# Kernel tuning notes

Measured on AMD Instinct MI355X. Metric: run time of the kernel, lower is better.

The kernel has to match this reference:

```python
import jax, jax.numpy as jnp
import numpy as np
import math

B, T, H, W, D = 64, 512, 128, 128, 32


def _lin(k, out, inn):
    k1, k2 = jax.random.split(k)
    lim = 1.0 / np.sqrt(inn)
    return (jax.random.uniform(k1, (out, inn), jnp.float32, -lim, lim),
            jax.random.uniform(k2, (out,), jnp.float32, -lim, lim))


def setup_inputs() -> dict:
    key = jax.random.key(0)
    ks = jax.random.split(key, 12)
    ts = jnp.broadcast_to(jnp.linspace(0.0, 4.0 * math.pi, T, dtype=jnp.float32), (B, T))
    coef = lambda k: jax.random.normal(k, (B, T - 1, D), jnp.float32) * 0.1
    i_W0, i_b0 = _lin(ks[4], W, D)
    i_W1, i_b1 = _lin(ks[5], W, W)
    i_W2, i_b2 = _lin(ks[6], H, W)
    f_W0, f_b0 = _lin(ks[7], W, H)
    f_W1, f_b1 = _lin(ks[8], W, W)
    f_W2, f_b2 = _lin(ks[9], H * D, W)
    l_W, l_b = _lin(ks[10], 1, H)
    return dict(ts=ts,
                coeff_d=coef(ks[0]), coeff_c=coef(ks[1]), coeff_b=coef(ks[2]), coeff_a=coef(ks[3]),
                i_W0=i_W0, i_b0=i_b0, i_W1=i_W1, i_b1=i_b1, i_W2=i_W2, i_b2=i_b2,
                f_W0=f_W0, f_b0=f_b0, f_W1=f_W1, f_b1=f_b1, f_W2=f_W2, f_b2=f_b2,
                l_W=l_W, l_b=l_b)


def reference(ts, coeff_d, coeff_c, coeff_b, coeff_a,
              i_W0, i_b0, i_W1, i_b1, i_W2, i_b2,
              f_W0, f_b0, f_W1, f_b1, f_W2, f_b2,
              l_W, l_b):
    def initial_mlp(x):  # eqx.nn.MLP default: relu hidden, identity final
        x = jax.nn.relu(i_W0 @ x + i_b0)
        x = jax.nn.relu(i_W1 @ x + i_b1)
        return i_W2 @ x + i_b2

    def func_mlp(y):  # softplus hidden, tanh final, reshape (H, D)
        h = jax.nn.softplus(f_W0 @ y + f_b0)
        h = jax.nn.softplus(f_W1 @ h + f_b1)
        return jnp.tanh(f_W2 @ h + f_b2).reshape(H, D)

    def single(ts_i, d, c, b, a):
        dt = ts_i[1] - ts_i[0]
        y0 = initial_mlp(a[0])  # control.evaluate(ts[0]) = a[0] (frac=0 in first interval)

        def deriv(t):  # diffrax CubicInterpolation.derivative
            idx = jnp.clip(jnp.searchsorted(ts_i, t, side='right') - 1, 0, ts_i.shape[0] - 2)
            frac = t - ts_i[idx]
            return b[idx] + frac * (2.0 * c[idx] + frac * 3.0 * d[idx])

        def f(t, y):  # ControlTerm.to_ode() vf_prod with control=dt
            return (func_mlp(y) @ deriv(t)) * dt

        def step(carry, _):  # ralston_step_fn
            t0, y = carry
            k1 = f(t0, y)
            k2 = f(t0 + 0.5 * dt, y + 0.5 * k1)
            k3 = f(t0 + 0.75 * dt, y + 0.75 * k2)
            y1 = (2.0 / 9.0 * k1 + 1.0 / 3.0 * k2 + 4.0 / 9.0 * k3) * dt + y
            return (t0 + dt, y1), y1

        _, ys = jax.lax.scan(step, (ts_i[0], y0), None, length=ts_i.shape[0])
        return jax.nn.sigmoid(ys @ l_W[0] + l_b[0])  # (T,), evolving_out=True

    return jax.vmap(single)(ts, coeff_d, coeff_c, coeff_b, coeff_a)
```

## Files before the change

### kernel.cpp

```cpp
#include <hip/hip_runtime.h>
#include <hip/hip_bf16.h>

#define TT 512
#define BB 64
#define HH 128
#define WW 128
#define DD 32
#define NTHR 512
#define CSTRIDE 16352

#define SMEM_BYTES 86016

typedef __attribute__((ext_vector_type(8))) short short8;
typedef __attribute__((ext_vector_type(4))) float f32x4;

__device__ __forceinline__ float softplus_f(float x) {
    return fmaxf(x, 0.f) + __logf(1.f + __expf(-fabsf(x)));
}
__device__ __forceinline__ float fast_tanh(float x) {
    float ax = fabsf(x);
    float e  = __expf(-2.f * ax);
    float r  = (1.f - e) * __builtin_amdgcn_rcpf(1.f + e);
    return copysignf(r, x);
}
__device__ __forceinline__ short bf16rne(float x) {
    unsigned u = __float_as_uint(x);
    u += 0x7fffu + ((u >> 16) & 1u);
    return (short)(u >> 16);
}
__device__ __forceinline__ void store_l2(unsigned long long* p, unsigned long long v) {
    asm volatile("global_store_dwordx2 %0, %1, off sc0"
                 :: "v"(p), "v"(v) : "memory");
}
__device__ __forceinline__ unsigned long long load_l2_atomic(unsigned long long* p) {
    unsigned long long v;
    asm volatile("global_atomic_add_x2 %0, %1, %2, off sc0\n\t"
                 "s_waitcnt vmcnt(0)"
                 : "=v"(v) : "v"(p), "v"(0ULL) : "memory");
    return v;
}

__global__ __launch_bounds__(NTHR, 2)
void cde_kernel(const float* __restrict__ ts,
                const float* __restrict__ cd, const float* __restrict__ cc,
                const float* __restrict__ cb, const float* __restrict__ ca,
                const float* __restrict__ iW0, const float* __restrict__ ib0,
                const float* __restrict__ iW1, const float* __restrict__ ib1,
                const float* __restrict__ iW2, const float* __restrict__ ib2,
                const float* __restrict__ fW0, const float* __restrict__ fb0,
                const float* __restrict__ fW1, const float* __restrict__ fb1,
                const float* __restrict__ fW2, const float* __restrict__ fb2,
                const float* __restrict__ lW, const float* __restrict__ lb,
                unsigned* __restrict__ xcdctr,
                float* camb,
                unsigned long long* kslow,
                float* __restrict__ out)
{
    extern __shared__ float sm[];
    float* tss    = sm;
    float* ybuf   = tss + TT;
    float* dvec   = ybuf + 128;
    float* scr    = dvec + 96;
    float* klocal = scr + 256;
    short* ybf    = (short*)(klocal + 32);
    short* h1bf   = ybf + 128;
    short* h2bf   = h1bf + 128;
    int*   clm    = (int*)(h2bf + 128);

    const int tid  = threadIdx.x;
    const int lane = tid & 63;
    const int wv   = tid >> 6;
    const int quad = lane >> 4;
    const int qr   = lane & 15;

    if (tid == 0) {
        unsigned xcc;
        asm volatile("s_getreg_b32 %0, hwreg(HW_REG_XCC_ID)" : "=s"(xcc));
        xcc &= 7u;
        unsigned slot = atomicAdd(&xcdctr[xcc], 1u);
        clm[0] = (int)(xcc * 8u + (slot >> 2));
        clm[1] = (int)(slot & 3u);
    }
    __syncthreads();
    const int b = clm[0];
    const int m = clm[1];

    unsigned long long* kfast =
        (unsigned long long*)(camb + (size_t)b * CSTRIDE + 2048);

    const int cg = qr & 3;
    const int ct = (qr >> 2) & 1;
    const int rh = qr >> 3;
    const int dbase = ct * 16 + quad * 4 + rh * 2;

    for (int i = tid; i < TT; i += NTHR) tss[i] = ts[(size_t)b * TT + i];

    short8 afr[4][8];
    #pragma unroll
    for (int gi = 0; gi < 4; ++gi) {
        int g = m * 32 + wv * 4 + gi;
        #pragma unroll
        for (int t = 0; t < 2; ++t)
        #pragma unroll
        for (int K = 0; K < 4; ++K) {
            int row = g * 32 + t * 16 + qr;
            int col = K * 32 + quad * 8;
            const float* src = fW2 + (size_t)row * WW + col;
            short8 v;
            #pragma unroll
            for (int j = 0; j < 8; ++j) v[j] = bf16rne(src[j]);
            afr[gi][t * 4 + K] = v;
        }
    }
    short8 w0f[4], w1f[4];
    #pragma unroll
    for (int K = 0; K < 4; ++K) {
        int row = wv * 16 + qr;
        int col = K * 32 + quad * 8;
        const float* s0 = fW0 + (size_t)row * HH + col;
        const float* s1 = fW1 + (size_t)row * WW + col;
        short8 v0, v1;
        #pragma unroll
        for (int j = 0; j < 8; ++j) { v0[j] = bf16rne(s0[j]); v1[j] = bf16rne(s1[j]); }
        w0f[K] = v0; w1f[K] = v1;
    }
    const float fb0r = fb0[wv * 16 + quad * 4 + cg];
    const float fb1r = fb1[wv * 16 + quad * 4 + cg];
    const int   hrow = m * 32 + wv * 4 + cg;
    const float fb2a = fb2[hrow * 32 + dbase];
    const float fb2b = fb2[hrow * 32 + dbase + 1];

    __syncthreads();

    const float dt = tss[1] - tss[0];
    float t00 = tss[0];
    const size_t cstride = (size_t)CSTRIDE;
    const float* cdb = cd + (size_t)b * cstride;
    const float* ccb = cc + (size_t)b * cstride;
    const float* cbb = cb + (size_t)b * cstride;

    if (tid < HH) {
        const float* a0 = ca + (size_t)b * cstride;
        float acc = ib0[tid];
        #pragma unroll
        for (int k = 0; k < DD; ++k) acc += iW0[tid * DD + k] * a0[k];
        scr[tid] = fmaxf(acc, 0.f);
    }
    __syncthreads();
    if (tid < HH) {
        float acc = ib1[tid];
        for (int k = 0; k < WW; ++k) acc += iW1[tid * WW + k] * scr[k];
        scr[128 + tid] = fmaxf(acc, 0.f);
    }
    __syncthreads();
    float yreg = 0.f, k1r = 0.f, k2r = 0.f;
    if (tid < HH) {
        float acc = ib2[tid];
        for (int k = 0; k < WW; ++k) acc += iW2[tid * WW + k] * scr[128 + k];
        yreg = acc;
        ybuf[tid] = acc;
        ybf[tid]  = bf16rne(acc);
    }
    __syncthreads();

    float lwa = 0.f, lwb = 0.f, lbv = 0.f;
    if (wv == 0) { lwa = lW[lane]; lwb = lW[64 + lane]; lbv = lb[0]; }

    for (int s = 0; s < TT; ++s) {
        if (wv < 3) {
            float tv = t00 + ((wv == 0) ? 0.f : (wv == 1) ? 0.5f : 0.75f) * dt;
            int cnt = 0;
            #pragma unroll
            for (int ch = 0; ch < 8; ++ch)
                cnt += __popcll(__ballot(tss[ch * 64 + lane] <= tv));
            int idx = min(max(cnt - 1, 0), TT - 2);
            if (lane < DD) {
                float frac = tv - tss[idx];
                size_t o = (size_t)idx * DD + lane;
                dvec[wv * 32 + lane] =
                    cbb[o] + frac * (2.f * ccb[o] + frac * 3.f * cdb[o]);
            }
        }

        #pragma unroll 1
        for (int q = 0; q < 3; ++q) {
            const int gen = s * 3 + q + 1;
            const int buf = gen & 1;

            {
                f32x4 aA = {0.f, 0.f, 0.f, 0.f}, aB = {0.f, 0.f, 0.f, 0.f};
                short8 b0 = *(const short8*)(ybf + 0 * 32 + quad * 8);
                short8 b1 = *(const short8*)(ybf + 1 * 32 + quad * 8);
                short8 b2 = *(const short8*)(ybf + 2 * 32 + quad * 8);
                short8 b3 = *(const short8*)(ybf + 3 * 32 + quad * 8);
                aA = __builtin_amdgcn_mfma_f32_16x16x32_bf16(w0f[0], b0, aA, 0, 0, 0);
                aB = __builtin_amdgcn_mfma_f32_16x16x32_bf16(w0f[1], b1, aB, 0, 0, 0);
                aA = __builtin_amdgcn_mfma_f32_16x16x32_bf16(w0f[2], b2, aA, 0, 0, 0);
                aB = __builtin_amdgcn_mfma_f32_16x16x32_bf16(w0f[3], b3, aB, 0, 0, 0);
                f32x4 h = aA + aB;
                if (qr < 4) {
                    float v = (qr & 1) ? ((qr & 2) ? h[3] : h[1])
                                       : ((qr & 2) ? h[2] : h[0]);
                    h1bf[wv * 16 + quad * 4 + qr] = bf16rne(softplus_f(v + fb0r));
                }
            }
            __syncthreads();
            {
                f32x4 aA = {0.f, 0.f, 0.f, 0.f}, aB = {0.f, 0.f, 0.f, 0.f};
                short8 b0 = *(const short8*)(h1bf + 0 * 32 + quad * 8);
                short8 b1 = *(const short8*)(h1bf + 1 * 32 + quad * 8);
                short8 b2 = *(const short8*)(h1bf + 2 * 32 + quad * 8);
                short8 b3 = *(const short8*)(h1bf + 3 * 32 + quad * 8);
                aA = __builtin_amdgcn_mfma_f32_16x16x32_bf16(w1f[0], b0, aA, 0, 0, 0);
                aB = __builtin_amdgcn_mfma_f32_16x16x32_bf16(w1f[1], b1, aB, 0, 0, 0);
                aA = __builtin_amdgcn_mfma_f32_16x16x32_bf16(w1f[2], b2, aA, 0, 0, 0);
                aB = __builtin_amdgcn_mfma_f32_16x16x32_bf16(w1f[3], b3, aB, 0, 0, 0);
                f32x4 h = aA + aB;
                if (qr < 4) {
                    float v = (qr & 1) ? ((qr & 2) ? h[3] : h[1])
                                       : ((qr & 2) ? h[2] : h[0]);
                    h2bf[wv * 16 + quad * 4 + qr] = bf16rne(softplus_f(v + fb1r));
                }
            }
            __syncthreads();

            {
                short8 bfr[4];
                #pragma unroll
                for (int K = 0; K < 4; ++K)
                    bfr[K] = *(const short8*)(h2bf + K * 32 + quad * 8);
                f32x4 A0[4], A1[4];
                #pragma unroll
                for (int gi = 0; gi < 4; ++gi) {
                    f32x4 a0 = {0.f, 0.f, 0.f, 0.f};
                    f32x4 a1 = {0.f, 0.f, 0.f, 0.f};
                    a0 = __builtin_amdgcn_mfma_f32_16x16x32_bf16(afr[gi][0], bfr[0], a0, 0, 0, 0);
                    a0 = __builtin_amdgcn_mfma_f32_16x16x32_bf16(afr[gi][1], bfr[1], a0, 0, 0, 0);
                    a0 = __builtin_amdgcn_mfma_f32_16x16x32_bf16(afr[gi][2], bfr[2], a0, 0, 0, 0);
                    a0 = __builtin_amdgcn_mfma_f32_16x16x32_bf16(afr[gi][3], bfr[3], a0, 0, 0, 0);
                    a1 = __builtin_amdgcn_mfma_f32_16x16x32_bf16(afr[gi][4], bfr[0], a1, 0, 0, 0);
                    a1 = __builtin_amdgcn_mfma_f32_16x16x32_bf16(afr[gi][5], bfr[1], a1, 0, 0, 0);
                    a1 = __builtin_amdgcn_mfma_f32_16x16x32_bf16(afr[gi][6], bfr[2], a1, 0, 0, 0);
                    a1 = __builtin_amdgcn_mfma_f32_16x16x32_bf16(afr[gi][7], bfr[3], a1, 0, 0, 0);
                    A0[gi] = a0; A1[gi] = a1;
                }
                f32x4 s0a = (cg & 1) ? A0[1] : A0[0];
                f32x4 s0b = (cg & 1) ? A0[3] : A0[2];
                f32x4 s0  = (cg & 2) ? s0b : s0a;
                f32x4 s1a = (cg & 1) ? A1[1] : A1[0];
                f32x4 s1b = (cg & 1) ? A1[3] : A1[2];
                f32x4 s1  = (cg & 2) ? s1b : s1a;
                f32x4 st  = ct ? s1 : s0;
                float va = rh ? st[2] : st[0];
                float vb = rh ? st[3] : st[1];
                float2 dv = *(const float2*)(dvec + q * 32 + dbase);
                float p = fast_tanh(va + fb2a) * dv.x + fast_tanh(vb + fb2b) * dv.y;
                p += __shfl_xor(p, 8);
                p += __shfl_xor(p, 4);
                p += __shfl_xor(p, 16);
                p += __shfl_xor(p, 32);
                if (lane < 4) {
                    const float kval = p * dt;
                    const size_t off = (size_t)buf * HH + m * 32 + wv * 4 + lane;
                    unsigned long long pk =
                        ((unsigned long long)__float_as_uint(kval) << 32) | (unsigned)gen;
                    klocal[wv * 4 + lane] = kval;
                    store_l2(kfast + off, pk);
                    __hip_atomic_store(&kslow[(size_t)(buf * BB + b) * HH + m * 32 + wv * 4 + lane],
                                       pk, __ATOMIC_RELAXED, __HIP_MEMORY_SCOPE_AGENT);
                }
            }
            __syncthreads();

            if (tid < HH) {
                float kv;
                const int rel = tid - m * 32;
                if (rel >= 0 && rel < 32) {
                    kv = klocal[rel];
                } else {
                    unsigned long long v;
                    int it = 0;
                    for (;;) {
                        if (it < 4 || (it & 1) == 0) {
                            v = load_l2_atomic(kfast + (size_t)buf * HH + tid);
                        } else {
                            v = __hip_atomic_load(&kslow[(size_t)(buf * BB + b) * HH + tid],
                                                  __ATOMIC_RELAXED, __HIP_MEMORY_SCOPE_AGENT);
                        }
                        if ((unsigned)v == (unsigned)gen) break;
                        if (++it > 64) __builtin_amdgcn_s_sleep(1);
                    }
                    kv = __uint_as_float((unsigned)(v >> 32));
                }
                float nxt;
                if (q == 0)      { k1r = kv; nxt = yreg + 0.5f  * kv; }
                else if (q == 1) { k2r = kv; nxt = yreg + 0.75f * kv; }
                else {
                    nxt = yreg + dt * ((2.f/9.f) * k1r + (1.f/3.f) * k2r + (4.f/9.f) * kv);
                    yreg = nxt;
                    ybuf[tid] = nxt;
                }
                ybf[tid] = bf16rne(nxt);
            }
            __syncthreads();
        }

        if (m == 0 && wv == 0) {
            float p = ybuf[lane] * lwa + ybuf[64 + lane] * lwb;
            p += __shfl_xor(p, 1);  p += __shfl_xor(p, 2);  p += __shfl_xor(p, 4);
            p += __shfl_xor(p, 8);  p += __shfl_xor(p, 16); p += __shfl_xor(p, 32);
            if (lane == 0) out[(size_t)b * TT + s] = 1.f / (1.f + __expf(-(p + lbv)));
        }
        t00 += dt;
    }
}

extern "C" void kernel_launch(void* const* d_in, const int* in_sizes, int n_in,
                              void* d_out, int out_size, void* d_ws, size_t ws_size,
                              hipStream_t stream) {
    const float* ts  = (const float*)d_in[0];
    const float* cdp = (const float*)d_in[1];
    const float* ccp = (const float*)d_in[2];
    const float* cbp = (const float*)d_in[3];
    const float* cap = (const float*)d_in[4];
    const float* iW0 = (const float*)d_in[5];
    const float* ib0 = (const float*)d_in[6];
    const float* iW1 = (const float*)d_in[7];
    const float* ib1 = (const float*)d_in[8];
    const float* iW2 = (const float*)d_in[9];
    const float* ib2 = (const float*)d_in[10];
    const float* fW0 = (const float*)d_in[11];
    const float* fb0 = (const float*)d_in[12];
    const float* fW1 = (const float*)d_in[13];
    const float* fb1 = (const float*)d_in[14];
    const float* fW2 = (const float*)d_in[15];
    const float* fb2 = (const float*)d_in[16];
    const float* lW  = (const float*)d_in[17];
    const float* lb  = (const float*)d_in[18];
    float* out = (float*)d_out;

    unsigned* xcdctr = (unsigned*)d_ws;
    unsigned long long* kslow = (unsigned long long*)((char*)d_ws + 256);
    hipMemsetAsync(d_ws, 0, 256 + (size_t)2 * BB * HH * sizeof(unsigned long long), stream);

    hipFuncSetAttribute((const void*)cde_kernel,
                        hipFuncAttributeMaxDynamicSharedMemorySize, SMEM_BYTES);
    hipLaunchKernelGGL(cde_kernel, dim3(256), dim3(NTHR), SMEM_BYTES, stream,
                       ts, cdp, ccp, cbp, cap, iW0, ib0, iW1, ib1, iW2, ib2,
                       fW0, fb0, fW1, fb1, fW2, fb2, lW, lb, xcdctr,
                       (float*)cap, kslow, out);
}
```

Before: 3.330 ms.

## Overlap cross-block k exchange with barrier and use lightweight LDS barriers

Replaces __syncthreads with an inline s_waitcnt lgkmcnt(0)+s_barrier so that outstanding global memory ops are not drained at each barrier. Consumers issue the first atomic probe of the foreign k value before the barrier and collect it afterwards, hiding part of the cross-block latency. The fallback kslow store is moved after the consumer step to get it off the critical path. The risk is memory-ordering subtleties, since global stores and loads are no longer fenced by the barrier.

```diff
diff --git a/kernel.cpp b/kernel.cpp
--- a/kernel.cpp
+++ b/kernel.cpp
@@ -28,6 +28,9 @@
     u += 0x7fffu + ((u >> 16) & 1u);
     return (short)(u >> 16);
 }
+__device__ __forceinline__ void lds_barrier() {
+    asm volatile("s_waitcnt lgkmcnt(0)\n\ts_barrier" ::: "memory");
+}
 __device__ __forceinline__ void store_l2(unsigned long long* p, unsigned long long v) {
     asm volatile("global_store_dwordx2 %0, %1, off sc0"
                  :: "v"(p), "v"(v) : "memory");
@@ -38,6 +41,13 @@
                  "s_waitcnt vmcnt(0)"
                  : "=v"(v) : "v"(p), "v"(0ULL) : "memory");
     return v;
+}
+__device__ __forceinline__ void probe_issue(unsigned long long* p, unsigned long long& v) {
+    asm volatile("global_atomic_add_x2 %0, %1, %2, off sc0"
+                 : "=v"(v) : "v"(p), "v"(0ULL) : "memory");
+}
+__device__ __forceinline__ void probe_collect(unsigned long long& v) {
+    asm volatile("s_waitcnt vmcnt(0)" : "+v"(v) :: "memory");
 }
 
 __global__ __launch_bounds__(NTHR, 2)
@@ -166,6 +176,10 @@
     float lwa = 0.f, lwb = 0.f, lbv = 0.f;
     if (wv == 0) { lwa = lW[lane]; lwb = lW[64 + lane]; lbv = lb[0]; }
 
+    const int rel = tid - m * 32;
+    const bool is_consumer = (tid < HH);
+    const bool is_foreign  = is_consumer && (rel < 0 || rel >= 32);
+
     for (int s = 0; s < TT; ++s) {
         if (wv < 3) {
             float tv = t00 + ((wv == 0) ? 0.f : (wv == 1) ? 0.5f : 0.75f) * dt;
@@ -204,7 +218,7 @@
                     h1bf[wv * 16 + quad * 4 + qr] = bf16rne(softplus_f(v + fb0r));
                 }
             }
-            __syncthreads();
+            lds_barrier();
             {
                 f32x4 aA = {0.f, 0.f, 0.f, 0.f}, aB = {0.f, 0.f, 0.f, 0.f};
                 short8 b0 = *(const short8*)(h1bf + 0 * 32 + quad * 8);
@@ -222,8 +236,9 @@
                     h2bf[wv * 16 + quad * 4 + qr] = bf16rne(softplus_f(v + fb1r));
                 }
             }
-            __syncthreads();
-
+            lds_barrier();
+
+            unsigned long long pksave = 0;
             {
                 short8 bfr[4];
                 #pragma unroll
@@ -262,33 +277,36 @@
                 if (lane < 4) {
                     const float kval = p * dt;
                     const size_t off = (size_t)buf * HH + m * 32 + wv * 4 + lane;
-                    unsigned long long pk =
-                        ((unsigned long long)__float_as_uint(kval) << 32) | (unsigned)gen;
+                    pksave = ((unsigned long long)__float_as_uint(kval) << 32)
+                           | (unsigned)gen;
                     klocal[wv * 4 + lane] = kval;
-                    store_l2(kfast + off, pk);
-                    __hip_atomic_store(&kslow[(size_t)(buf * BB + b) * HH + m * 32 + wv * 4 + lane],
-                                       pk, __ATOMIC_RELAXED, __HIP_MEMORY_SCOPE_AGENT);
-                }
-            }
-            __syncthreads();
-
-            if (tid < HH) {
+                    store_l2(kfast + off, pksave);
+                }
+            }
+
+            unsigned long long vprobe = 0;
+            unsigned long long* fp = kfast + (size_t)buf * HH + tid;
+            if (is_foreign) probe_issue(fp, vprobe);
+
+            lds_barrier();
+
+            if (is_consumer) {
                 float kv;
-                const int rel = tid - m * 32;
-                if (rel >= 0 && rel < 32) {
+                if (!is_foreign) {
                     kv = klocal[rel];
                 } else {
-                    unsigned long long v;
+                    probe_collect(vprobe);
+                    unsigned long long v = vprobe;
                     int it = 0;
-                    for (;;) {
-                        if (it < 4 || (it & 1) == 0) {
-                            v = load_l2_atomic(kfast + (size_t)buf * HH + tid);
+                    while ((unsigned)v != (unsigned)gen) {
+                        ++it;
+                        if (it < 6 || (it & 1) == 0) {
+                            v = load_l2_atomic(fp);
                         } else {
                             v = __hip_atomic_load(&kslow[(size_t)(buf * BB + b) * HH + tid],
                                                   __ATOMIC_RELAXED, __HIP_MEMORY_SCOPE_AGENT);
                         }
-                        if ((unsigned)v == (unsigned)gen) break;
-                        if (++it > 64) __builtin_amdgcn_s_sleep(1);
+                        if (it > 64) __builtin_amdgcn_s_sleep(1);
                     }
                     kv = __uint_as_float((unsigned)(v >> 32));
                 }
@@ -302,7 +320,13 @@
                 }
                 ybf[tid] = bf16rne(nxt);
             }
-            __syncthreads();
+
+            if (lane < 4) {
+                __hip_atomic_store(&kslow[(size_t)(buf * BB + b) * HH + m * 32 + wv * 4 + lane],
+                                   pksave, __ATOMIC_RELAXED, __HIP_MEMORY_SCOPE_AGENT);
+            }
+
+            lds_barrier();
         }
 
         if (m == 0 && wv == 0) {
```

New measurement: 3.557 ms. 1.07x slower.
